# Kernel tuning notes

Measured on AMD Instinct MI355X. Metric: run time of the kernel, lower is better.

The kernel has to match this reference:

```python
import jax, jax.numpy as jnp
import numpy as np

N_CELLS = 10   # nr_cells
CELL = 20      # cell_size (w)
R = 1          # read heads
HID = 128      # controller hidden
IN = 10        # dnc input_size
OUT = 10       # output_dim
CLIP = 20.0
IFACE = R * CELL + 3 * CELL + 5 * R + 3  # 88


def _lstm_step(x, h, c, Wih, Whh, b):
    gates = x @ Wih.T + h @ Whh.T + b
    i, f, g, o = jnp.split(gates, 4, axis=-1)
    c = jax.nn.sigmoid(f) * c + jax.nn.sigmoid(i) * jnp.tanh(g)
    h = jax.nn.sigmoid(o) * jnp.tanh(c)
    return h, c


def _content(mem, keys, strengths):
    # mem (b,n,w), keys (b,k,w), strengths (b,k) -> (b,k,n)
    dot = jnp.einsum('bkw,bnw->bkn', keys, mem)
    kn = jnp.linalg.norm(keys, axis=-1, keepdims=True)
    mn = jnp.linalg.norm(mem, axis=-1)[:, None, :]
    return jax.nn.softmax(dot / (kn * mn + 1e-6) * strengths[..., None], axis=-1)


def _allocate(usage):
    u = 1e-6 + (1.0 - 1e-6) * usage
    idx = jnp.argsort(u, axis=-1)                      # ascending usage
    su = jnp.take_along_axis(u, idx, axis=-1)
    excl = jnp.concatenate([jnp.ones_like(su[:, :1]), jnp.cumprod(su, axis=-1)[:, :-1]], axis=-1)
    sa = (1.0 - su) * excl                             # sorted allocation weights
    inv = jnp.argsort(idx, axis=-1)
    return jnp.take_along_axis(sa, inv, axis=-1)


def _dnc_forward(x, W_ih0, W_hh0, b0, W_ih1, W_hh1, b1, W_if, b_if, W_out, b_out):
    B, T, _ = x.shape
    dt = x.dtype
    z = lambda *s: jnp.zeros(s, dt)
    carry0 = (z(B, HID), z(B, HID), z(B, HID), z(B, HID),   # h0,c0,h1,c1
              z(B, N_CELLS, CELL),                          # memory
              z(B, N_CELLS),                                # usage
              z(B, N_CELLS),                                # precedence
              z(B, N_CELLS, N_CELLS),                       # link matrix
              z(B, R, N_CELLS),                             # read weights
              z(B, N_CELLS),                                # write weights
              z(B, R, CELL))                                # read vectors
    eye = jnp.eye(N_CELLS, dtype=dt)

    def step(carry, xt):
        h0, c0, h1, c1, mem, usage, prec, link, rw, ww, rv = carry
        inp = jnp.concatenate([xt, rv.reshape(B, R * CELL)], axis=-1)
        h0, c0 = _lstm_step(inp, h0, c0, W_ih0, W_hh0, b0)
        h1, c1 = _lstm_step(h0, h1, c1, W_ih1, W_hh1, b1)
        ctrl = jnp.clip(h1, -CLIP, CLIP)
        xi = ctrl @ W_if.T + b_if                            # (B, 88)
        rk = jnp.tanh(xi[:, 0:20]).reshape(B, R, CELL)       # read keys
        rs = jax.nn.softplus(xi[:, 20:21])                   # read strengths
        wk = jnp.tanh(xi[:, 21:41]).reshape(B, 1, CELL)      # write key
        ws = jax.nn.softplus(xi[:, 41:42])                   # write strength
        er = jax.nn.sigmoid(xi[:, 42:62])                    # erase vector
        wv = jnp.tanh(xi[:, 62:82])                          # write vector
        fg = jax.nn.sigmoid(xi[:, 82:83])                    # free gates
        ga = jax.nn.sigmoid(xi[:, 83:84])                    # allocation gate
        gw = jax.nn.sigmoid(xi[:, 84:85])                    # write gate
        modes = jax.nn.softmax(xi[:, 85:88].reshape(B, R, 3), axis=-1)
        # --- write ---
        psi = jnp.prod(1.0 - fg[:, :, None] * rw, axis=1)    # retention (b,n)
        usage = (usage + ww - usage * ww) * psi
        alloc = _allocate(usage)
        cw = _content(mem, wk, ws)[:, 0]                     # (b,n)
        ww = gw * (ga * alloc + (1.0 - ga) * cw)
        mem = mem * (1.0 - ww[:, :, None] * er[:, None, :]) + ww[:, :, None] * wv[:, None, :]
        link = (1.0 - ww[:, :, None] - ww[:, None, :]) * link + ww[:, :, None] * prec[:, None, :]
        link = link * (1.0 - eye)
        prec = (1.0 - ww.sum(-1, keepdims=True)) * prec + ww
        # --- read ---
        fwd_w = jnp.einsum('brn,bmn->brm', rw, link)         # L @ w  (forward)
        bwd_w = jnp.einsum('brn,bnm->brm', rw, link)         # L^T @ w (backward)
        cr = _content(mem, rk, rs)
        rw = modes[..., 0:1] * bwd_w + modes[..., 1:2] * cr + modes[..., 2:3] * fwd_w
        rv = jnp.einsum('brn,bnw->brw', rw, mem)
        o = jnp.concatenate([ctrl, rv.reshape(B, R * CELL)], axis=-1)
        y = o @ W_out.T + b_out
        return (h0, c0, h1, c1, mem, usage, prec, link, rw, ww, rv), y

    _, ys = jax.lax.scan(step, carry0, jnp.swapaxes(x, 0, 1))
    return ys[-1]  # output[:, -1, :]


def setup_inputs() -> dict:
    key = jax.random.key(0)
    ks = jax.random.split(key, 8)
    s = 0.08
    B, T = 512, 512
    return {
        'x': jax.random.normal(ks[0], (B, T, IN), jnp.float32),
        'W_ih0': s * jax.random.normal(ks[1], (4 * HID, IN + R * CELL), jnp.float32),
        'W_hh0': s * jax.random.normal(ks[2], (4 * HID, HID), jnp.float32),
        'b0': jnp.zeros((4 * HID,), jnp.float32),
        'W_ih1': s * jax.random.normal(ks[3], (4 * HID, HID), jnp.float32),
        'W_hh1': s * jax.random.normal(ks[4], (4 * HID, HID), jnp.float32),
        'b1': jnp.zeros((4 * HID,), jnp.float32),
        'W_if': s * jax.random.normal(ks[5], (IFACE, HID), jnp.float32),
        'b_if': jnp.zeros((IFACE,), jnp.float32),
        'W_out': s * jax.random.normal(ks[6], (OUT, HID + R * CELL), jnp.float32),
        'b_out': jnp.zeros((OUT,), jnp.float32),
    }


def reference(x, W_ih0, W_hh0, b0, W_ih1, W_hh1, b1, W_if, b_if, W_out, b_out):
    return _dnc_forward(x, W_ih0, W_hh0, b0, W_ih1, W_hh1, b1, W_if, b_if, W_out, b_out)
```

## Files before the change

### kernel.cpp

```cpp
#include <hip/hip_runtime.h>
#include <math.h>

#define NT 512
#define NB 512
#define HID 128
#define NIN 10
#define NC 10
#define CW 20
#define NIF 88
#define NOUT 10
#define GB 2
#define BLK 512

typedef _Float16 h1;
typedef _Float16 h2 __attribute__((ext_vector_type(2)));

__device__ __forceinline__ float rcpf(float x) { return __builtin_amdgcn_rcpf(x); }
__device__ __forceinline__ float sigf(float x) { return rcpf(1.0f + __expf(-x)); }
__device__ __forceinline__ float tanhf_(float x) {
  float xc = fminf(fmaxf(x, -15.f), 15.f);
  float e = __expf(2.f * xc);
  return (e - 1.f) * rcpf(e + 1.f);
}
__device__ __forceinline__ float splus(float x) { return fmaxf(x, 0.0f) + __logf(1.f + __expf(-fabsf(x))); }

__device__ __forceinline__ float dot2(h2 a, h2 b, float c) {
#if __has_builtin(__builtin_amdgcn_fdot2)
  return __builtin_amdgcn_fdot2(a, b, c, false);
#else
  c += (float)a.x * (float)b.x;
  c += (float)a.y * (float)b.y;
  return c;
#endif
}

#define LDSFENCE() do { asm volatile("s_waitcnt lgkmcnt(0)" ::: "memory"); \
                        __builtin_amdgcn_sched_barrier(0); } while (0)

#define BC(f) __builtin_bit_cast(h2, f)

#define DOTF4(W, fa, fb)                                   \
  a0 = dot2(BC((W).x), BC((fa).x), a0);                    \
  a1 = dot2(BC((W).x), BC((fb).x), a1);                    \
  a2 = dot2(BC((W).y), BC((fa).y), a2);                    \
  a3 = dot2(BC((W).y), BC((fb).y), a3);                    \
  a0 = dot2(BC((W).z), BC((fa).z), a0);                    \
  a1 = dot2(BC((W).z), BC((fb).z), a1);                    \
  a2 = dot2(BC((W).w), BC((fa).w), a2);                    \
  a3 = dot2(BC((W).w), BC((fb).w), a3);

#define LSTEP(W, i, Pa, Pb) { float4 fa = (Pa)[i], fb = (Pb)[i]; DOTF4(W, fa, fb) }

__device__ __forceinline__ float4 pack8(const float* p) {
  h2 v0, v1, v2, v3;
  v0.x=(h1)p[0]; v0.y=(h1)p[1]; v1.x=(h1)p[2]; v1.y=(h1)p[3];
  v2.x=(h1)p[4]; v2.y=(h1)p[5]; v3.x=(h1)p[6]; v3.y=(h1)p[7];
  float4 r;
  r.x=__builtin_bit_cast(float,v0); r.y=__builtin_bit_cast(float,v1);
  r.z=__builtin_bit_cast(float,v2); r.w=__builtin_bit_cast(float,v3);
  return r;
}

__global__ __launch_bounds__(256) void dnc_pack_kernel(
    const float* __restrict__ Wih1, const float* __restrict__ Whh1, float4* __restrict__ ws)
{
  int i = blockIdx.x * 256 + threadIdx.x;
  if (i < 16*512) {
    int c = i >> 9, rr = i & 511;
    ws[i] = pack8(Whh1 + (size_t)rr*HID + 8*c);
  } else if (i < 18*512) {
    int j = i - 16*512; int c2 = j >> 9, rr = j & 511;
    ws[i] = pack8(Wih1 + (size_t)rr*HID + (14 + c2)*8);
  }
}

__global__ __launch_bounds__(BLK)
void dnc_olap_kernel(
    const float* __restrict__ x,
    const float* __restrict__ Wih0, const float* __restrict__ Whh0, const float* __restrict__ b0,
    const float* __restrict__ Wih1, const float* __restrict__ Whh1, const float* __restrict__ b1,
    const float* __restrict__ Wif,  const float* __restrict__ bif,
    const float* __restrict__ Wout, const float* __restrict__ bout,
    const float4* __restrict__ wsT,
    float* __restrict__ out)
{
  __shared__ __align__(16) float4 s_wih1T[14][512];
  __shared__ __align__(16) float4 s_wifT[16*89];
  __shared__ __align__(16) float s_g[GB][512];
  __shared__ __align__(16) float s_fp[NIF][9];
  __shared__ float s_bif[NIF];
  __shared__ __align__(16) h1   s_xbuf[2][GB][16];
  __shared__ __align__(16) h1   s_rvh[GB][24];
  __shared__ __align__(16) h1   s_h0h[GB][HID];
  __shared__ __align__(16) h1   s_h1h[GB][HID];
  __shared__ __align__(16) h1   s_ctrlh[GB][HID];
  __shared__ __align__(16) float s_ctrl[GB][HID];
  __shared__ __align__(16) float s_mem[GB][NC][CW];
  __shared__ float s_rk[GB][CW], s_wk[GB][CW], s_er[GB][CW], s_wv[GB][CW];
  __shared__ float s_mraw[GB][3];
  __shared__ float s_sc[GB][8];
  __shared__ float s_usage[GB][NC], s_u[GB][NC];
  __shared__ float s_prec[GB][NC], s_prec2[GB][NC];
  __shared__ float s_link[GB][NC][NC];
  __shared__ float s_rw[GB][NC], s_ww[GB][NC];
  __shared__ float s_rv[GB][CW];
  __shared__ float s_cw[GB][NC], s_cr[GB][NC], s_fwd[GB][NC], s_bwd[GB][NC];

  const int tid = threadIdx.x;
  const int bg  = blockIdx.x * GB;
  const int r   = tid;

  float4 A0,A1,A2,A3,A4;
  float4 B0,B1,B2,B3,B4,B5,B6,B7,B8,B9,B10,B11,B12,B13,B14,B15;
  float b0r, b1r;
  {
    const float* p = Wih0 + (size_t)r * (NIN + CW);
    A0 = pack8(p);
    { h2 v0,z; v0.x=(h1)p[8]; v0.y=(h1)p[9]; z.x=(h1)0.f; z.y=(h1)0.f;
      float4 f; f.x=__builtin_bit_cast(float,v0); f.y=__builtin_bit_cast(float,z);
      f.z=f.y; f.w=f.y; A1=f; }
    A2 = pack8(p+10); A3 = pack8(p+18);
    { h2 v0,v1,z; v0.x=(h1)p[26]; v0.y=(h1)p[27]; v1.x=(h1)p[28]; v1.y=(h1)p[29];
      z.x=(h1)0.f; z.y=(h1)0.f;
      float4 f; f.x=__builtin_bit_cast(float,v0); f.y=__builtin_bit_cast(float,v1);
      f.z=__builtin_bit_cast(float,z); f.w=f.z; A4=f; }
    const float* q0 = Whh0 + (size_t)r*HID;
    B0 =pack8(q0);    B1 =pack8(q0+8);  B2 =pack8(q0+16);  B3 =pack8(q0+24);
    B4 =pack8(q0+32); B5 =pack8(q0+40); B6 =pack8(q0+48);  B7 =pack8(q0+56);
    B8 =pack8(q0+64); B9 =pack8(q0+72); B10=pack8(q0+80);  B11=pack8(q0+88);
    B12=pack8(q0+96); B13=pack8(q0+104);B14=pack8(q0+112); B15=pack8(q0+120);
    b0r = b0[r]; b1r = b1[r];
  }

  for (int idx = tid; idx < 14*512; idx += BLK) {
    int c = idx >> 9, rr = idx & 511;
    s_wih1T[c][rr] = pack8(Wih1 + (size_t)rr*HID + 8*c);
  }
  for (int idx = tid; idx < 16*NIF; idx += BLK) {
    int j = idx / NIF, q = idx - j*NIF;
    s_wifT[j*89 + q] = pack8(Wif + (size_t)q*HID + 8*j);
  }
  if (tid < NIF) s_bif[tid] = bif[tid];

  if (tid < GB*HID) { int b=tid>>7, j=tid&127;
    s_h0h[b][j]=(h1)0.f; s_h1h[b][j]=(h1)0.f; s_ctrlh[b][j]=(h1)0.f; s_ctrl[b][j]=0.f; }
  for (int i = tid; i < GB*NC*CW; i += BLK) { int b=i/(NC*CW), e=i%(NC*CW);
    s_mem[b][e/CW][e%CW]=0.f; }
  for (int i = tid; i < GB*NC*NC; i += BLK) { int b=i/(NC*NC), e=i%(NC*NC);
    s_link[b][e/NC][e%NC]=0.f; }
  if (tid < GB*NC) { int b=tid/NC, n=tid%NC;
    s_usage[b][n]=0.f; s_prec[b][n]=0.f; s_rw[b][n]=0.f; s_ww[b][n]=0.f; }
  if (tid < GB*CW) { int b=tid/CW, c=tid%CW; s_rv[b][c]=0.f; }
  if (tid < GB*24) { int b=tid/24, c=tid%24; s_rvh[b][c]=(h1)0.f; }
  if (tid < 2*GB*16) { int u=tid, d=u>>5, b=(u>>4)&1, i=u&15;
    float v = 0.f;
    if (d == 0 && i < NIN) v = x[((size_t)(bg+b)*NT + 0)*NIN + i];
    s_xbuf[d][b][i] = (h1)v;
  }
  float c0r = 0.f, c1r = 0.f;
  __syncthreads();

  auto dnc_tail = [&](int lane) {
    #pragma unroll
    for (int e = lane; e < 2*NIF; e += 64) {
      int b = e & 1, q = e >> 1;
      float a = s_bif[q];
      #pragma unroll
      for (int c = 0; c < 4; ++c) a += s_fp[q][2*c+b];
      if      (q < 20)  s_rk[b][q]    = tanhf_(a);
      else if (q == 20) s_sc[b][0]    = splus(a);
      else if (q < 41)  s_wk[b][q-21] = tanhf_(a);
      else if (q == 41) s_sc[b][1]    = splus(a);
      else if (q < 62)  s_er[b][q-42] = sigf(a);
      else if (q < 82)  s_wv[b][q-62] = tanhf_(a);
      else if (q == 82) s_sc[b][2]    = sigf(a);
      else if (q == 83) s_sc[b][3]    = sigf(a);
      else if (q == 84) s_sc[b][4]    = sigf(a);
      else              s_mraw[b][q-85] = a;
    }
    LDSFENCE();

    if (lane < GB*NC) {
      int b = lane/NC, n = lane%NC;
      float fg = s_sc[b][2];
      float psi = 1.f - fg * s_rw[b][n];
      float u = s_usage[b][n], w = s_ww[b][n];
      u = (u + w - u*w) * psi;
      s_usage[b][n] = u;
      s_u[b][n] = 1e-6f + (1.0f - 1e-6f) * u;
      float dot=0.f, mn=0.f, kn=0.f;
      #pragma unroll
      for (int c = 0; c < CW; ++c) {
        float m = s_mem[b][n][c], k = s_wk[b][c];
        dot += k*m; mn += m*m; kn += k*k;
      }
      s_cw[b][n] = dot * rcpf(sqrtf(kn)*sqrtf(mn) + 1e-6f) * s_sc[b][1];
    } else if (lane < GB*NC + GB) {
      int b = lane - GB*NC;
      float m0=s_mraw[b][0], m1=s_mraw[b][1], m2=s_mraw[b][2];
      float mm = fmaxf(m0, fmaxf(m1, m2));
      float e0=__expf(m0-mm), e1=__expf(m1-mm), e2=__expf(m2-mm);
      float es = rcpf(e0+e1+e2);
      s_sc[b][5]=e0*es; s_sc[b][6]=e1*es; s_sc[b][7]=e2*es;
    }
    LDSFENCE();

    if (lane < GB*NC) {
      int b = lane/NC, n = lane%NC;
      float mx = -1e30f;
      #pragma unroll
      for (int m = 0; m < NC; ++m) mx = fmaxf(mx, s_cw[b][m]);
      float sm = 0.f;
      #pragma unroll
      for (int m = 0; m < NC; ++m) sm += __expf(s_cw[b][m]-mx);
      float cwv = __expf(s_cw[b][n]-mx) * rcpf(sm);
      float un = s_u[b][n];
      float excl = 1.f;
      #pragma unroll
      for (int m = 0; m < NC; ++m) {
        float um = s_u[b][m];
        bool before = (um < un) || (um == un && m < n);
        excl *= before ? um : 1.f;
      }
      float alloc = (1.f - un) * excl;
      float ga = s_sc[b][3], gw = s_sc[b][4];
      s_ww[b][n] = gw * (ga*alloc + (1.f-ga)*cwv);
    }
    LDSFENCE();

    #pragma unroll
    for (int e = lane; e < GB*NC*CW; e += 64) {
      int b = e/(NC*CW), rr = (e%(NC*CW))/CW, c = e%CW;
      float w = s_ww[b][rr];
      s_mem[b][rr][c] = s_mem[b][rr][c] * (1.f - w*s_er[b][c]) + w*s_wv[b][c];
    }
    #pragma unroll
    for (int e = lane; e < GB*NC*NC; e += 64) {
      int b = e/(NC*NC), i = (e%(NC*NC))/NC, j = e%NC;
      float wi = s_ww[b][i], wj = s_ww[b][j];
      float l = (1.f - wi - wj)*s_link[b][i][j] + wi*s_prec[b][j];
      s_link[b][i][j] = (i==j) ? 0.f : l;
    }
    if (lane < GB*NC) {
      int b = lane/NC, n = lane%NC;
      float sw2 = 0.f;
      #pragma unroll
      for (int m = 0; m < NC; ++m) sw2 += s_ww[b][m];
      s_prec2[b][n] = (1.f - sw2)*s_prec[b][n] + s_ww[b][n];
    }
    LDSFENCE();

    if (lane < GB*NC) {
      int b = lane/NC, m = lane%NC;
      s_prec[b][m] = s_prec2[b][m];
      float a = 0.f;
      #pragma unroll
      for (int n = 0; n < NC; ++n) a += s_rw[b][n]*s_link[b][m][n];
      s_fwd[b][m] = a;
    } else if (lane < 2*GB*NC) {
      int q = lane - GB*NC, b = q/NC, m = q%NC;
      float a = 0.f;
      #pragma unroll
      for (int n = 0; n < NC; ++n) a += s_rw[b][n]*s_link[b][n][m];
      s_bwd[b][m] = a;
    } else if (lane < 3*GB*NC) {
      int q = lane - 2*GB*NC, b = q/NC, n = q%NC;
      float dot=0.f, mn=0.f, kn=0.f;
      #pragma unroll
      for (int c = 0; c < CW; ++c) {
        float m = s_mem[b][n][c], k = s_rk[b][c];
        dot += k*m; mn += m*m; kn += k*k;
      }
      s_cr[b][n] = dot * rcpf(sqrtf(kn)*sqrtf(mn)+1e-6f) * s_sc[b][0];
    }
    LDSFENCE();

    if (lane < GB*NC) {
      int b = lane/NC, n = lane%NC;
      float mx = -1e30f;
      #pragma unroll
      for (int m = 0; m < NC; ++m) mx = fmaxf(mx, s_cr[b][m]);
      float sm = 0.f;
      #pragma unroll
      for (int m = 0; m < NC; ++m) sm += __expf(s_cr[b][m]-mx);
      float cr = __expf(s_cr[b][n]-mx)*rcpf(sm);
      s_rw[b][n] = s_sc[b][5]*s_bwd[b][n] + s_sc[b][6]*cr + s_sc[b][7]*s_fwd[b][n];
    }
    LDSFENCE();

    if (lane < GB*CW) {
      int b = lane/CW, c = lane%CW;
      float a = 0.f;
      #pragma unroll
      for (int n = 0; n < NC; ++n) a += s_rw[b][n]*s_mem[b][n][c];
      s_rv[b][c] = a;
      s_rvh[b][c] = (h1)a;
    }
  };

  for (int t = 0; t < NT; ++t) {
    if (tid >= 448) {
      const int lane = tid - 448;
      float xv = 0.f;
      if (lane < GB*NIN && (t+1) < NT) {
        int b = lane/NIN, i = lane%NIN;
        xv = x[((size_t)(bg+b)*NT + (t+1))*NIN + i];
      }
      if (t > 0) dnc_tail(lane);
      if (lane < GB*NIN && (t+1) < NT) {
        int b = lane/NIN, i = lane%NIN;
        s_xbuf[(t+1)&1][b][i] = (h1)xv;
      }
    }
    unsigned lnd = 0;
    asm volatile("" : "+v"(lnd));
    const float4* WS = (const float4*)((const char*)wsT + lnd);
    float4 u0 = WS[0*512+tid], u1 = WS[1*512+tid];
    float4 t0 = WS[2*512+tid], t1 = WS[3*512+tid];
    float r0a, r0b, g1a, g1b;
    {
      float a0=b0r, a1=b0r, a2=0.f, a3=0.f;
      const float4* Xa = (const float4*)&s_xbuf[t&1][0][0];
      const float4* Xb = (const float4*)&s_xbuf[t&1][1][0];
      LSTEP(A0,0,Xa,Xb) LSTEP(A1,1,Xa,Xb)
      const float4* Ha = (const float4*)s_h0h[0];
      const float4* Hb = (const float4*)s_h0h[1];
      LSTEP(B0,0,Ha,Hb)   LSTEP(B1,1,Ha,Hb)   LSTEP(B2,2,Ha,Hb)   LSTEP(B3,3,Ha,Hb)
      LSTEP(B4,4,Ha,Hb)   LSTEP(B5,5,Ha,Hb)   LSTEP(B6,6,Ha,Hb)   LSTEP(B7,7,Ha,Hb)
      LSTEP(B8,8,Ha,Hb)   LSTEP(B9,9,Ha,Hb)   LSTEP(B10,10,Ha,Hb) LSTEP(B11,11,Ha,Hb)
      LSTEP(B12,12,Ha,Hb) LSTEP(B13,13,Ha,Hb) LSTEP(B14,14,Ha,Hb) LSTEP(B15,15,Ha,Hb)
      r0a = a0+a2; r0b = a1+a3;
    }
    {
      float a0=0.f, a1=0.f, a2=0.f, a3=0.f;
      const float4* Ga = (const float4*)s_h1h[0];
      const float4* Gb = (const float4*)s_h1h[1];
      LSTEP(u0, 0,Ga,Gb) LSTEP(u1, 1,Ga,Gb)
      u0 = WS[ 4*512+tid]; u1 = WS[ 5*512+tid];
      LSTEP(t0, 2,Ga,Gb) LSTEP(t1, 3,Ga,Gb)
      t0 = WS[ 6*512+tid]; t1 = WS[ 7*512+tid];
      LSTEP(u0, 4,Ga,Gb) LSTEP(u1, 5,Ga,Gb)
      u0 = WS[ 8*512+tid]; u1 = WS[ 9*512+tid];
      LSTEP(t0, 6,Ga,Gb) LSTEP(t1, 7,Ga,Gb)
      t0 = WS[10*512+tid]; t1 = WS[11*512+tid];
      LSTEP(u0, 8,Ga,Gb) LSTEP(u1, 9,Ga,Gb)
      u0 = WS[12*512+tid]; u1 = WS[13*512+tid];
      LSTEP(t0,10,Ga,Gb) LSTEP(t1,11,Ga,Gb)
      t0 = WS[14*512+tid]; t1 = WS[15*512+tid];
      LSTEP(u0,12,Ga,Gb) LSTEP(u1,13,Ga,Gb)
      LSTEP(t0,14,Ga,Gb) LSTEP(t1,15,Ga,Gb)
      g1a = a0+a2; g1b = a1+a3;
    }
    __syncthreads();

    {
      float a0=r0a, a1=r0b, a2=0.f, a3=0.f;
      const float4* Ra = (const float4*)&s_rvh[0][0];
      const float4* Rb = (const float4*)&s_rvh[1][0];
      LSTEP(A2,0,Ra,Rb) LSTEP(A3,1,Ra,Rb) LSTEP(A4,2,Ra,Rb)
      s_g[0][r] = a0+a2; s_g[1][r] = a1+a3;
    }
    __syncthreads();

    if (tid < GB*HID) {
      int b = tid>>7, j = tid&127;
      float gi=s_g[b][j], gf=s_g[b][HID+j], gg=s_g[b][2*HID+j], go=s_g[b][3*HID+j];
      float c = sigf(gf)*c0r + sigf(gi)*tanhf_(gg);
      c0r = c;
      float h = sigf(go)*tanhf_(c);
      s_h0h[b][j] = (h1)h;
    }
    __syncthreads();

    {
      float4 v0 = WS[16*512+tid], v1 = WS[17*512+tid];
      float a0 = g1a + b1r, a1 = g1b + b1r, a2=0.f, a3=0.f;
      const float4* Ha = (const float4*)s_h0h[0];
      const float4* Hb = (const float4*)s_h0h[1];
      { float4 w=s_wih1T[ 0][r]; LSTEP(w, 0,Ha,Hb) }
      { float4 w=s_wih1T[ 1][r]; LSTEP(w, 1,Ha,Hb) }
      { float4 w=s_wih1T[ 2][r]; LSTEP(w, 2,Ha,Hb) }
      { float4 w=s_wih1T[ 3][r]; LSTEP(w, 3,Ha,Hb) }
      { float4 w=s_wih1T[ 4][r]; LSTEP(w, 4,Ha,Hb) }
      { float4 w=s_wih1T[ 5][r]; LSTEP(w, 5,Ha,Hb) }
      { float4 w=s_wih1T[ 6][r]; LSTEP(w, 6,Ha,Hb) }
      { float4 w=s_wih1T[ 7][r]; LSTEP(w, 7,Ha,Hb) }
      { float4 w=s_wih1T[ 8][r]; LSTEP(w, 8,Ha,Hb) }
      { float4 w=s_wih1T[ 9][r]; LSTEP(w, 9,Ha,Hb) }
      { float4 w=s_wih1T[10][r]; LSTEP(w,10,Ha,Hb) }
      { float4 w=s_wih1T[11][r]; LSTEP(w,11,Ha,Hb) }
      { float4 w=s_wih1T[12][r]; LSTEP(w,12,Ha,Hb) }
      { float4 w=s_wih1T[13][r]; LSTEP(w,13,Ha,Hb) }
      LSTEP(v0,14,Ha,Hb) LSTEP(v1,15,Ha,Hb)
      s_g[0][r] = a0+a2; s_g[1][r] = a1+a3;
    }
    __syncthreads();

    if (tid < GB*HID) {
      int b = tid>>7, j = tid&127;
      float gi=s_g[b][j], gf=s_g[b][HID+j], gg=s_g[b][2*HID+j], go=s_g[b][3*HID+j];
      float c = sigf(gf)*c1r + sigf(gi)*tanhf_(gg);
      c1r = c;
      float h = sigf(go)*tanhf_(c);
      float ctl = fminf(fmaxf(h, -20.f), 20.f);
      s_h1h[b][j] = (h1)h;
      s_ctrl[b][j] = ctl;
      s_ctrlh[b][j] = (h1)ctl;
    }
    __syncthreads();

    if (tid < 4*NIF) {
      int q = tid >> 2, c = tid & 3;
      float a0=0.f, a1=0.f, a2=0.f, a3=0.f;
      const float4* Ca = (const float4*)s_ctrlh[0];
      const float4* Cb = (const float4*)s_ctrlh[1];
      float4 w0 = s_wifT[(4*c+0)*89 + q];
      float4 w1 = s_wifT[(4*c+1)*89 + q];
      float4 w2 = s_wifT[(4*c+2)*89 + q];
      float4 w3 = s_wifT[(4*c+3)*89 + q];
      LSTEP(w0, 4*c+0, Ca, Cb) LSTEP(w1, 4*c+1, Ca, Cb)
      LSTEP(w2, 4*c+2, Ca, Cb) LSTEP(w3, 4*c+3, Ca, Cb)
      s_fp[q][2*c  ] = a0+a2;
      s_fp[q][2*c+1] = a1+a3;
    }
    __syncthreads();
  }

  if (tid >= 448) dnc_tail(tid - 448);
  __syncthreads();

  if (tid < GB*NOUT) {
    int b = tid/NOUT, o = tid%NOUT;
    float a = bout[o];
    const float* Wr = Wout + o*(HID+CW);
    #pragma unroll 4
    for (int k = 0; k < HID; ++k) a += Wr[k]*s_ctrl[b][k];
    #pragma unroll
    for (int c = 0; c < CW; ++c) a += Wr[HID+c]*s_rv[b][c];
    out[(size_t)(bg+b)*NOUT + o] = a;
  }
}

extern "C" void kernel_launch(void* const* d_in, const int* in_sizes, int n_in,
                              void* d_out, int out_size, void* d_ws, size_t ws_size,
                              hipStream_t stream) {
  (void)in_sizes; (void)n_in; (void)out_size; (void)ws_size;
  const float* x    = (const float*)d_in[0];
  const float* Wih0 = (const float*)d_in[1];
  const float* Whh0 = (const float*)d_in[2];
  const float* b0   = (const float*)d_in[3];
  const float* Wih1 = (const float*)d_in[4];
  const float* Whh1 = (const float*)d_in[5];
  const float* b1   = (const float*)d_in[6];
  const float* Wif  = (const float*)d_in[7];
  const float* bif  = (const float*)d_in[8];
  const float* Wout = (const float*)d_in[9];
  const float* bout = (const float*)d_in[10];
  float* out = (float*)d_out;
  float4* ws = (float4*)d_ws;

  dnc_pack_kernel<<<dim3(36), dim3(256), 0, stream>>>(Wih1, Whh1, ws);
  dnc_olap_kernel<<<dim3(NB/GB), dim3(BLK), 0, stream>>>(
      x, Wih0, Whh0, b0, Wih1, Whh1, b1, Wif, bif, Wout, bout, ws, out);
}
```

Baseline: 6.119 ms.

## Interleave gate rows per quad and combine LSTM gates via ds_swizzle

Gate rows are permuted so each group of four consecutive threads holds the i,f,g,o gates of one hidden unit. ds_swizzle broadcasts within the quad, so the LSTM cell update runs in registers right after the matvec. This removes the s_g LDS round trip and two block-wide barriers per layer per timestep. The DNC tail work is also split so two waves each handle one batch element at raised priority, at the cost of redundant cell math across the four lanes of a quad.

```diff
diff --git a/kernel.cpp b/kernel.cpp
--- a/kernel.cpp
+++ b/kernel.cpp
@@ -34,6 +34,11 @@
 #endif
 }
 
+__device__ __forceinline__ float bq0(float v) { return __builtin_bit_cast(float, __builtin_amdgcn_ds_swizzle(__builtin_bit_cast(int, v), 0x001C)); }
+__device__ __forceinline__ float bq1(float v) { return __builtin_bit_cast(float, __builtin_amdgcn_ds_swizzle(__builtin_bit_cast(int, v), 0x003C)); }
+__device__ __forceinline__ float bq2(float v) { return __builtin_bit_cast(float, __builtin_amdgcn_ds_swizzle(__builtin_bit_cast(int, v), 0x005C)); }
+__device__ __forceinline__ float bq3(float v) { return __builtin_bit_cast(float, __builtin_amdgcn_ds_swizzle(__builtin_bit_cast(int, v), 0x007C)); }
+
 #define LDSFENCE() do { asm volatile("s_waitcnt lgkmcnt(0)" ::: "memory"); \
                         __builtin_amdgcn_sched_barrier(0); } while (0)
 
@@ -61,21 +66,20 @@
   return r;
 }
 
+__device__ __host__ __forceinline__ int rowmap(int s) { return (s & 3) * 128 + (s >> 2); }
+
 __global__ __launch_bounds__(256) void dnc_pack_kernel(
     const float* __restrict__ Wih1, const float* __restrict__ Whh1, float4* __restrict__ ws)
 {
   int i = blockIdx.x * 256 + threadIdx.x;
-  if (i < 16*512) {
-    int c = i >> 9, rr = i & 511;
-    ws[i] = pack8(Whh1 + (size_t)rr*HID + 8*c);
-  } else if (i < 18*512) {
-    int j = i - 16*512; int c2 = j >> 9, rr = j & 511;
-    ws[i] = pack8(Wih1 + (size_t)rr*HID + (14 + c2)*8);
-  }
+  int s = i & 511, c = i >> 9;
+  int R = rowmap(s);
+  if (c < 16)      ws[i] = pack8(Whh1 + (size_t)R*HID + 8*c);
+  else if (c < 18) ws[i] = pack8(Wih1 + (size_t)R*HID + (14 + (c-16))*8);
 }
 
 __global__ __launch_bounds__(BLK)
-void dnc_olap_kernel(
+void dnc_quad_kernel(
     const float* __restrict__ x,
     const float* __restrict__ Wih0, const float* __restrict__ Whh0, const float* __restrict__ b0,
     const float* __restrict__ Wih1, const float* __restrict__ Whh1, const float* __restrict__ b1,
@@ -86,7 +90,6 @@
 {
   __shared__ __align__(16) float4 s_wih1T[14][512];
   __shared__ __align__(16) float4 s_wifT[16*89];
-  __shared__ __align__(16) float s_g[GB][512];
   __shared__ __align__(16) float s_fp[NIF][9];
   __shared__ float s_bif[NIF];
   __shared__ __align__(16) h1   s_xbuf[2][GB][16];
@@ -108,13 +111,13 @@
 
   const int tid = threadIdx.x;
   const int bg  = blockIdx.x * GB;
-  const int r   = tid;
+  const int R   = rowmap(tid);
 
   float4 A0,A1,A2,A3,A4;
   float4 B0,B1,B2,B3,B4,B5,B6,B7,B8,B9,B10,B11,B12,B13,B14,B15;
   float b0r, b1r;
   {
-    const float* p = Wih0 + (size_t)r * (NIN + CW);
+    const float* p = Wih0 + (size_t)R * (NIN + CW);
     A0 = pack8(p);
     { h2 v0,z; v0.x=(h1)p[8]; v0.y=(h1)p[9]; z.x=(h1)0.f; z.y=(h1)0.f;
       float4 f; f.x=__builtin_bit_cast(float,v0); f.y=__builtin_bit_cast(float,z);
@@ -124,17 +127,17 @@
       z.x=(h1)0.f; z.y=(h1)0.f;
       float4 f; f.x=__builtin_bit_cast(float,v0); f.y=__builtin_bit_cast(float,v1);
       f.z=__builtin_bit_cast(float,z); f.w=f.z; A4=f; }
-    const float* q0 = Whh0 + (size_t)r*HID;
+    const float* q0 = Whh0 + (size_t)R*HID;
     B0 =pack8(q0);    B1 =pack8(q0+8);  B2 =pack8(q0+16);  B3 =pack8(q0+24);
     B4 =pack8(q0+32); B5 =pack8(q0+40); B6 =pack8(q0+48);  B7 =pack8(q0+56);
     B8 =pack8(q0+64); B9 =pack8(q0+72); B10=pack8(q0+80);  B11=pack8(q0+88);
     B12=pack8(q0+96); B13=pack8(q0+104);B14=pack8(q0+112); B15=pack8(q0+120);
-    b0r = b0[r]; b1r = b1[r];
+    b0r = b0[R]; b1r = b1[R];
   }
 
   for (int idx = tid; idx < 14*512; idx += BLK) {
-    int c = idx >> 9, rr = idx & 511;
-    s_wih1T[c][rr] = pack8(Wih1 + (size_t)rr*HID + 8*c);
+    int c = idx >> 9, s = idx & 511;
+    s_wih1T[c][s] = pack8(Wih1 + (size_t)rowmap(s)*HID + 8*c);
   }
   for (int idx = tid; idx < 16*NIF; idx += BLK) {
     int j = idx / NIF, q = idx - j*NIF;
@@ -157,13 +160,12 @@
     if (d == 0 && i < NIN) v = x[((size_t)(bg+b)*NT + 0)*NIN + i];
     s_xbuf[d][b][i] = (h1)v;
   }
-  float c0r = 0.f, c1r = 0.f;
+  float c0rA = 0.f, c0rB = 0.f, c1rA = 0.f, c1rB = 0.f;
   __syncthreads();
 
-  auto dnc_tail = [&](int lane) {
+  auto dnc_tail = [&](int b, int lane) {
     #pragma unroll
-    for (int e = lane; e < 2*NIF; e += 64) {
-      int b = e & 1, q = e >> 1;
+    for (int q = lane; q < NIF; q += 64) {
       float a = s_bif[q];
       #pragma unroll
       for (int c = 0; c < 4; ++c) a += s_fp[q][2*c+b];
@@ -180,8 +182,8 @@
     }
     LDSFENCE();
 
-    if (lane < GB*NC) {
-      int b = lane/NC, n = lane%NC;
+    if (lane < NC) {
+      int n = lane;
       float fg = s_sc[b][2];
       float psi = 1.f - fg * s_rw[b][n];
       float u = s_usage[b][n], w = s_ww[b][n];
@@ -195,8 +197,7 @@
         dot += k*m; mn += m*m; kn += k*k;
       }
       s_cw[b][n] = dot * rcpf(sqrtf(kn)*sqrtf(mn) + 1e-6f) * s_sc[b][1];
-    } else if (lane < GB*NC + GB) {
-      int b = lane - GB*NC;
+    } else if (lane == NC) {
       float m0=s_mraw[b][0], m1=s_mraw[b][1], m2=s_mraw[b][2];
       float mm = fmaxf(m0, fmaxf(m1, m2));
       float e0=__expf(m0-mm), e1=__expf(m1-mm), e2=__expf(m2-mm);
@@ -205,8 +206,8 @@
     }
     LDSFENCE();
 
-    if (lane < GB*NC) {
-      int b = lane/NC, n = lane%NC;
+    if (lane < NC) {
+      int n = lane;
       float mx = -1e30f;
       #pragma unroll
       for (int m = 0; m < NC; ++m) mx = fmaxf(mx, s_cw[b][m]);
@@ -229,20 +230,20 @@
     LDSFENCE();
 
     #pragma unroll
-    for (int e = lane; e < GB*NC*CW; e += 64) {
-      int b = e/(NC*CW), rr = (e%(NC*CW))/CW, c = e%CW;
+    for (int e = lane; e < NC*CW; e += 64) {
+      int rr = e/CW, c = e%CW;
       float w = s_ww[b][rr];
       s_mem[b][rr][c] = s_mem[b][rr][c] * (1.f - w*s_er[b][c]) + w*s_wv[b][c];
     }
     #pragma unroll
-    for (int e = lane; e < GB*NC*NC; e += 64) {
-      int b = e/(NC*NC), i = (e%(NC*NC))/NC, j = e%NC;
+    for (int e = lane; e < NC*NC; e += 64) {
+      int i = e/NC, j = e%NC;
       float wi = s_ww[b][i], wj = s_ww[b][j];
       float l = (1.f - wi - wj)*s_link[b][i][j] + wi*s_prec[b][j];
       s_link[b][i][j] = (i==j) ? 0.f : l;
     }
-    if (lane < GB*NC) {
-      int b = lane/NC, n = lane%NC;
+    if (lane < NC) {
+      int n = lane;
       float sw2 = 0.f;
       #pragma unroll
       for (int m = 0; m < NC; ++m) sw2 += s_ww[b][m];
@@ -250,21 +251,21 @@
     }
     LDSFENCE();
 
-    if (lane < GB*NC) {
-      int b = lane/NC, m = lane%NC;
+    if (lane < NC) {
+      int m = lane;
       s_prec[b][m] = s_prec2[b][m];
       float a = 0.f;
       #pragma unroll
       for (int n = 0; n < NC; ++n) a += s_rw[b][n]*s_link[b][m][n];
       s_fwd[b][m] = a;
-    } else if (lane < 2*GB*NC) {
-      int q = lane - GB*NC, b = q/NC, m = q%NC;
+    } else if (lane < 2*NC) {
+      int m = lane - NC;
       float a = 0.f;
       #pragma unroll
       for (int n = 0; n < NC; ++n) a += s_rw[b][n]*s_link[b][n][m];
       s_bwd[b][m] = a;
-    } else if (lane < 3*GB*NC) {
-      int q = lane - 2*GB*NC, b = q/NC, n = q%NC;
+    } else if (lane < 3*NC) {
+      int n = lane - 2*NC;
       float dot=0.f, mn=0.f, kn=0.f;
       #pragma unroll
       for (int c = 0; c < CW; ++c) {
@@ -275,8 +276,8 @@
     }
     LDSFENCE();
 
-    if (lane < GB*NC) {
-      int b = lane/NC, n = lane%NC;
+    if (lane < NC) {
+      int n = lane;
       float mx = -1e30f;
       #pragma unroll
       for (int m = 0; m < NC; ++m) mx = fmaxf(mx, s_cr[b][m]);
@@ -288,8 +289,8 @@
     }
     LDSFENCE();
 
-    if (lane < GB*CW) {
-      int b = lane/CW, c = lane%CW;
+    if (lane < CW) {
+      int c = lane;
       float a = 0.f;
       #pragma unroll
       for (int n = 0; n < NC; ++n) a += s_rw[b][n]*s_mem[b][n][c];
@@ -299,18 +300,19 @@
   };
 
   for (int t = 0; t < NT; ++t) {
-    if (tid >= 448) {
-      const int lane = tid - 448;
+    const int wv = tid >> 6;
+    if (wv >= 6) {
+      const int lane = tid & 63, b = wv - 6;
       float xv = 0.f;
-      if (lane < GB*NIN && (t+1) < NT) {
-        int b = lane/NIN, i = lane%NIN;
-        xv = x[((size_t)(bg+b)*NT + (t+1))*NIN + i];
-      }
-      if (t > 0) dnc_tail(lane);
-      if (lane < GB*NIN && (t+1) < NT) {
-        int b = lane/NIN, i = lane%NIN;
-        s_xbuf[(t+1)&1][b][i] = (h1)xv;
-      }
+      if (lane >= 32 && lane < 32+NIN && (t+1) < NT)
+        xv = x[((size_t)(bg+b)*NT + (t+1))*NIN + (lane-32)];
+      if (t > 0) {
+        __builtin_amdgcn_s_setprio(1);
+        dnc_tail(b, lane);
+        __builtin_amdgcn_s_setprio(0);
+      }
+      if (lane >= 32 && lane < 32+NIN && (t+1) < NT)
+        s_xbuf[(t+1)&1][b][lane-32] = (h1)xv;
     }
     unsigned lnd = 0;
     asm volatile("" : "+v"(lnd));
@@ -358,17 +360,18 @@
       const float4* Ra = (const float4*)&s_rvh[0][0];
       const float4* Rb = (const float4*)&s_rvh[1][0];
       LSTEP(A2,0,Ra,Rb) LSTEP(A3,1,Ra,Rb) LSTEP(A4,2,Ra,Rb)
-      s_g[0][r] = a0+a2; s_g[1][r] = a1+a3;
-    }
-    __syncthreads();
-
-    if (tid < GB*HID) {
-      int b = tid>>7, j = tid&127;
-      float gi=s_g[b][j], gf=s_g[b][HID+j], gg=s_g[b][2*HID+j], go=s_g[b][3*HID+j];
-      float c = sigf(gf)*c0r + sigf(gi)*tanhf_(gg);
-      c0r = c;
-      float h = sigf(go)*tanhf_(c);
-      s_h0h[b][j] = (h1)h;
+      float gA = a0+a2, gB = a1+a3;
+      float giA=bq0(gA), gfA=bq1(gA), ggA=bq2(gA), goA=bq3(gA);
+      float giB=bq0(gB), gfB=bq1(gB), ggB=bq2(gB), goB=bq3(gB);
+      float cA = sigf(gfA)*c0rA + sigf(giA)*tanhf_(ggA);
+      float cB = sigf(gfB)*c0rB + sigf(giB)*tanhf_(ggB);
+      c0rA = cA; c0rB = cB;
+      float hA = sigf(goA)*tanhf_(cA);
+      float hB = sigf(goB)*tanhf_(cB);
+      if ((tid & 3) == 0) {
+        int u = tid >> 2;
+        s_h0h[0][u] = (h1)hA; s_h0h[1][u] = (h1)hB;
+      }
     }
     __syncthreads();
 
@@ -377,35 +380,37 @@
       float a0 = g1a + b1r, a1 = g1b + b1r, a2=0.f, a3=0.f;
       const float4* Ha = (const float4*)s_h0h[0];
       const float4* Hb = (const float4*)s_h0h[1];
-      { float4 w=s_wih1T[ 0][r]; LSTEP(w, 0,Ha,Hb) }
-      { float4 w=s_wih1T[ 1][r]; LSTEP(w, 1,Ha,Hb) }
-      { float4 w=s_wih1T[ 2][r]; LSTEP(w, 2,Ha,Hb) }
-      { float4 w=s_wih1T[ 3][r]; LSTEP(w, 3,Ha,Hb) }
-      { float4 w=s_wih1T[ 4][r]; LSTEP(w, 4,Ha,Hb) }
-      { float4 w=s_wih1T[ 5][r]; LSTEP(w, 5,Ha,Hb) }
-      { float4 w=s_wih1T[ 6][r]; LSTEP(w, 6,Ha,Hb) }
-      { float4 w=s_wih1T[ 7][r]; LSTEP(w, 7,Ha,Hb) }
-      { float4 w=s_wih1T[ 8][r]; LSTEP(w, 8,Ha,Hb) }
-      { float4 w=s_wih1T[ 9][r]; LSTEP(w, 9,Ha,Hb) }
-      { float4 w=s_wih1T[10][r]; LSTEP(w,10,Ha,Hb) }
-      { float4 w=s_wih1T[11][r]; LSTEP(w,11,Ha,Hb) }
-      { float4 w=s_wih1T[12][r]; LSTEP(w,12,Ha,Hb) }
-      { float4 w=s_wih1T[13][r]; LSTEP(w,13,Ha,Hb) }
+      { float4 w=s_wih1T[ 0][tid]; LSTEP(w, 0,Ha,Hb) }
+      { float4 w=s_wih1T[ 1][tid]; LSTEP(w, 1,Ha,Hb) }
+      { float4 w=s_wih1T[ 2][tid]; LSTEP(w, 2,Ha,Hb) }
+      { float4 w=s_wih1T[ 3][tid]; LSTEP(w, 3,Ha,Hb) }
+      { float4 w=s_wih1T[ 4][tid]; LSTEP(w, 4,Ha,Hb) }
+      { float4 w=s_wih1T[ 5][tid]; LSTEP(w, 5,Ha,Hb) }
+      { float4 w=s_wih1T[ 6][tid]; LSTEP(w, 6,Ha,Hb) }
+      { float4 w=s_wih1T[ 7][tid]; LSTEP(w, 7,Ha,Hb) }
+      { float4 w=s_wih1T[ 8][tid]; LSTEP(w, 8,Ha,Hb) }
+      { float4 w=s_wih1T[ 9][tid]; LSTEP(w, 9,Ha,Hb) }
+      { float4 w=s_wih1T[10][tid]; LSTEP(w,10,Ha,Hb) }
+      { float4 w=s_wih1T[11][tid]; LSTEP(w,11,Ha,Hb) }
+      { float4 w=s_wih1T[12][tid]; LSTEP(w,12,Ha,Hb) }
+      { float4 w=s_wih1T[13][tid]; LSTEP(w,13,Ha,Hb) }
       LSTEP(v0,14,Ha,Hb) LSTEP(v1,15,Ha,Hb)
-      s_g[0][r] = a0+a2; s_g[1][r] = a1+a3;
-    }
-    __syncthreads();
-
-    if (tid < GB*HID) {
-      int b = tid>>7, j = tid&127;
-      float gi=s_g[b][j], gf=s_g[b][HID+j], gg=s_g[b][2*HID+j], go=s_g[b][3*HID+j];
-      float c = sigf(gf)*c1r + sigf(gi)*tanhf_(gg);
-      c1r = c;
-      float h = sigf(go)*tanhf_(c);
-      float ctl = fminf(fmaxf(h, -20.f), 20.f);
-      s_h1h[b][j] = (h1)h;
-      s_ctrl[b][j] = ctl;
-      s_ctrlh[b][j] = (h1)ctl;
+      float gA = a0+a2, gB = a1+a3;
+      float giA=bq0(gA), gfA=bq1(gA), ggA=bq2(gA), goA=bq3(gA);
+      float giB=bq0(gB), gfB=bq1(gB), ggB=bq2(gB), goB=bq3(gB);
+      float cA = sigf(gfA)*c1rA + sigf(giA)*tanhf_(ggA);
+      float cB = sigf(gfB)*c1rB + sigf(giB)*tanhf_(ggB);
+      c1rA = cA; c1rB = cB;
+      float hA = sigf(goA)*tanhf_(cA);
+      float hB = sigf(goB)*tanhf_(cB);
+      float clA = fminf(fmaxf(hA, -20.f), 20.f);
+      float clB = fminf(fmaxf(hB, -20.f), 20.f);
+      if ((tid & 3) == 0) {
+        int u = tid >> 2;
+        s_h1h[0][u] = (h1)hA;  s_h1h[1][u] = (h1)hB;
+        s_ctrl[0][u] = clA;    s_ctrl[1][u] = clB;
+        s_ctrlh[0][u] = (h1)clA; s_ctrlh[1][u] = (h1)clB;
+      }
     }
     __syncthreads();
 
@@ -426,7 +431,7 @@
     __syncthreads();
   }
 
-  if (tid >= 448) dnc_tail(tid - 448);
+  if ((tid >> 6) >= 6) dnc_tail((tid >> 6) - 6, tid & 63);
   __syncthreads();
 
   if (tid < GB*NOUT) {
@@ -460,6 +465,6 @@
   float4* ws = (float4*)d_ws;
 
   dnc_pack_kernel<<<dim3(36), dim3(256), 0, stream>>>(Wih1, Whh1, ws);
-  dnc_olap_kernel<<<dim3(NB/GB), dim3(BLK), 0, stream>>>(
+  dnc_quad_kernel<<<dim3(NB/GB), dim3(BLK), 0, stream>>>(
       x, Wih0, Whh0, b0, Wih1, Whh1, b1, Wif, bif, Wout, bout, ws, out);
 }
```

After: 6.428 ms. 5.1% more time.
